# Kernel optimization log

Hardware: AMD Instinct MI355X
Metric: run time of the kernel (lower is better)

## Reference

```python
import jax, jax.numpy as jnp
import numpy as np

MAXDISP = 128  # from init_kwargs; 3*MAXDISP == 384 == enc0 in_planes

# 24 census offsets in a 5x5 window (center (2,2) skipped), order as in torch source
OFFSETS = [(0,0),(1,0),(2,0),(3,0),(4,0),(0,1),(1,1),(2,1),(3,1),(4,1),
           (0,2),(1,2),(3,2),(4,2),(0,3),(1,3),(2,3),(3,3),(4,3),
           (0,4),(1,4),(2,4),(3,4),(4,4)]


def rgb_to_ycbcr(img):
    # img: (n,3,h,w)
    r, g, b = img[:, 0], img[:, 1], img[:, 2]
    y = 0.299 * r + 0.587 * g + 0.114 * b
    cb = (b - y) * 0.564 + 0.5
    cr = (r - y) * 0.713 + 0.5
    return jnp.stack([y, cb, cr], axis=1)


def avg_pool2(x):
    n, c, h, w = x.shape
    return x.reshape(n, c, h // 2, 2, w // 2, 2).mean(axis=(3, 5))


def census5(img):
    # img: (n,1,h,w) float -> (n,1,h,w) int32, 24-bit census code, 2px zero border
    n, c, h, w = img.shape
    center = img[:, :, 2:h - 2, 2:w - 2]
    # (24, n, 1, h-4, w-4) boolean comparisons, exactly the torch offset order
    bits = jnp.stack([(img[:, :, v:v + h - 4, u:u + w - 4] >= center)
                      for (u, v) in OFFSETS], axis=0).astype(jnp.int32)
    weights = (2 ** jnp.arange(23, -1, -1)).astype(jnp.int32)  # census = census*2 + bit fold
    cen = jnp.tensordot(weights, bits, axes=1)
    return jnp.pad(cen, ((0, 0), (0, 0), (2, 2), (2, 2)))


def cost_volume(l, r, maxdisp, op):
    # l, r: (n,1,h,w). out[:, d, :, x] = op(l[x+d], r[x]) for x < w-d else 0,
    # matching torch's slice (left[d:w] vs right[0:w-d]) + right-pad with zeros.
    w = l.shape[-1]
    xs = jnp.arange(w)

    def per_d(d):
        l_sh = jnp.roll(l, -d, axis=-1)          # l_sh[..., x] = l[..., x+d] (wrapped part masked)
        c = op(l_sh, r)
        return jnp.where(xs < w - d, c, jnp.zeros_like(c))

    cv = jax.vmap(per_d)(jnp.arange(maxdisp))    # (D, n, 1, h, w)
    return cv[:, :, 0].transpose(1, 0, 2, 3)     # (n, D, h, w)


def setup_inputs() -> dict:
    key = jax.random.key(0)
    k1, k2 = jax.random.split(key)
    left = jax.random.uniform(k1, (2, 3, 384, 1280), dtype=jnp.float32)
    right = jax.random.uniform(k2, (2, 3, 384, 1280), dtype=jnp.float32)
    return {"left": left, "right": right}


def reference(left, right):
    # FDSCS front-end: half-res YCbCr, census+Hamming on Y, abs-diff on Cb/Cr, unify
    lp, rp = avg_pool2(left), avg_pool2(right)
    lyuv, ryuv = rgb_to_ycbcr(lp), rgb_to_ycbcr(rp)

    lc = census5(lyuv[:, 0:1])
    rc = census5(ryuv[:, 0:1])
    # Hamming distance = popcount of 24-bit XOR (codes < 2^24, so popcount == 24-bit loop)
    ham = cost_volume(lc, rc, MAXDISP,
                      lambda a, b: jax.lax.population_count(jnp.bitwise_xor(a, b))
                      ).astype(jnp.float32)
    u = cost_volume(lyuv[:, 1:2], ryuv[:, 1:2], MAXDISP, lambda a, b: jnp.abs(a - b))
    v = cost_volume(lyuv[:, 2:3], ryuv[:, 2:3], MAXDISP, lambda a, b: jnp.abs(a - b))

    # Unify_size normalization constants from torch source
    y_n = (ham - 11.08282948) / 0.1949711
    u_n = (u - 0.02175535) / 35.91432953
    v_n = (v - 0.02679042) / 26.79782867
    return jnp.concatenate([y_n, u_n, v_n], axis=1)  # (n, 3*MAXDISP, h/2, w/2)
```

## Files before the change

kernel.cpp:

```cpp
#include <hip/hip_runtime.h>

#define H   384
#define W   1280
#define PH  192
#define PW  640
#define PP  (PH*PW)

typedef float f32x4 __attribute__((ext_vector_type(4)));
typedef int   i32x4 __attribute__((ext_vector_type(4)));

__global__ __launch_bounds__(256) void pool_ycbcr_kernel(
    const float* __restrict__ left, const float* __restrict__ right,
    float* __restrict__ yp, float* __restrict__ cbp, float* __restrict__ crp)
{
    int tid = blockIdx.x * blockDim.x + threadIdx.x;
    if (tid >= 4 * PP) return;
    int p   = tid / PP;
    int rem = tid - p * PP;
    int y   = rem / PW;
    int x   = rem - y * PW;

    const float* src = (p < 2 ? left : right) + (size_t)(p & 1) * 3 * H * W;

    float pc[3];
#pragma unroll
    for (int c = 0; c < 3; ++c) {
        const float* ch = src + (size_t)c * H * W + (size_t)(2 * y) * W + 2 * x;
        float2 a = *(const float2*)ch;
        float2 b = *(const float2*)(ch + W);
        float s = __fadd_rn(__fadd_rn(__fadd_rn(a.x, a.y), b.x), b.y);
        pc[c] = __fmul_rn(s, 0.25f);
    }
    float yv = __fadd_rn(__fadd_rn(__fmul_rn(0.299f, pc[0]),
                                   __fmul_rn(0.587f, pc[1])),
                         __fmul_rn(0.114f, pc[2]));
    float cb = __fadd_rn(__fmul_rn(__fsub_rn(pc[2], yv), 0.564f), 0.5f);
    float cr = __fadd_rn(__fmul_rn(__fsub_rn(pc[0], yv), 0.713f), 0.5f);

    yp[tid]  = yv;
    cbp[tid] = cb;
    crp[tid] = cr;
}

__global__ __launch_bounds__(256) void census_kernel(
    const float* __restrict__ yp, int* __restrict__ cen)
{
    int tid = blockIdx.x * blockDim.x + threadIdx.x;
    if (tid >= 4 * PP) return;
    int p   = tid / PP;
    int rem = tid - p * PP;
    int y   = rem / PW;
    int x   = rem - y * PW;

    int code = 0;
    if (y >= 2 && y < PH - 2 && x >= 2 && x < PW - 2) {
        const float* base = yp + (size_t)p * PP;
        float c = base[y * PW + x];
        int bit = 23;
#pragma unroll
        for (int v = 0; v < 5; ++v) {
#pragma unroll
            for (int u = 0; u < 5; ++u) {
                if (u == 2 && v == 2) continue;
                float nb = base[(y - 2 + v) * PW + (x - 2 + u)];
                code |= (nb >= c ? 1 : 0) << bit;
                --bit;
            }
        }
    }
    cen[tid] = code;
}

__global__ __launch_bounds__(256) void costvol_kernel(
    const float* __restrict__ cbp, const float* __restrict__ crp,
    const int* __restrict__ cen, float* __restrict__ out)
{
    const float m1 = 11.08282948f, i1 = 1.0f / 0.1949711f;
    const float m2 = 0.02175535f,  i2 = 1.0f / 35.91432953f;
    const float m3 = 0.02679042f,  i3 = 1.0f / 26.79782867f;

    int b  = (blockIdx.x & 7) * 768 + (blockIdx.x >> 3);

    int yt = b & 7;
    int t  = b >> 3;
    int n  = t / 384;
    int ch = t - n * 384;
    int g  = ch >> 7;
    int d  = ch & 127;
    int nvalid = PW - d;
    int y0 = yt * 24;
    int s  = d & 3;
    int dal = d - s;
    const int tid = threadIdx.x;

    f32x4* ob = (f32x4*)(out + (((size_t)(n * 384 + ch)) * PH + y0) * PW);

    if (g == 0) {
        const float c0 = (0.0f - m1) * i1;
        const int* L = cen + (size_t)n * PP;
        const int* R = cen + (size_t)(2 + n) * PP;
#pragma unroll 5
        for (int k = 0; k < 15; ++k) {
            int i  = tid + 256 * k;
            int yy = i / 160;
            int x0 = (i - yy * 160) * 4;
            int row = (y0 + yy) * PW;
            i32x4 rv = *(const i32x4*)(R + row + x0);
            const int* Lp = L + row + x0 + dal;
            i32x4 A  = *(const i32x4*)(Lp);
            i32x4 Bv = *(const i32x4*)(Lp + 4);
            int e0, e1, e2, e3;
            if      (s == 0) { e0 = A.x;  e1 = A.y;  e2 = A.z;  e3 = A.w;  }
            else if (s == 1) { e0 = A.y;  e1 = A.z;  e2 = A.w;  e3 = Bv.x; }
            else if (s == 2) { e0 = A.z;  e1 = A.w;  e2 = Bv.x; e3 = Bv.y; }
            else             { e0 = A.w;  e1 = Bv.x; e2 = Bv.y; e3 = Bv.z; }
            f32x4 ov;
            ov.x = (x0 + 0 < nvalid) ? ((float)__popc(e0 ^ rv.x) - m1) * i1 : c0;
            ov.y = (x0 + 1 < nvalid) ? ((float)__popc(e1 ^ rv.y) - m1) * i1 : c0;
            ov.z = (x0 + 2 < nvalid) ? ((float)__popc(e2 ^ rv.z) - m1) * i1 : c0;
            ov.w = (x0 + 3 < nvalid) ? ((float)__popc(e3 ^ rv.w) - m1) * i1 : c0;
            __builtin_nontemporal_store(ov, ob + i);
        }
    } else {
        const float m  = (g == 1) ? m2 : m3;
        const float iv = (g == 1) ? i2 : i3;
        const float c0 = (0.0f - m) * iv;
        const float* P = (g == 1) ? cbp : crp;
        const float* L = P + (size_t)n * PP;
        const float* R = P + (size_t)(2 + n) * PP;
#pragma unroll 5
        for (int k = 0; k < 15; ++k) {
            int i  = tid + 256 * k;
            int yy = i / 160;
            int x0 = (i - yy * 160) * 4;
            int row = (y0 + yy) * PW;
            f32x4 rv = *(const f32x4*)(R + row + x0);
            const float* Lp = L + row + x0 + dal;
            f32x4 A  = *(const f32x4*)(Lp);
            f32x4 Bv = *(const f32x4*)(Lp + 4);
            float e0, e1, e2, e3;
            if      (s == 0) { e0 = A.x;  e1 = A.y;  e2 = A.z;  e3 = A.w;  }
            else if (s == 1) { e0 = A.y;  e1 = A.z;  e2 = A.w;  e3 = Bv.x; }
            else if (s == 2) { e0 = A.z;  e1 = A.w;  e2 = Bv.x; e3 = Bv.y; }
            else             { e0 = A.w;  e1 = Bv.x; e2 = Bv.y; e3 = Bv.z; }
            f32x4 ov;
            ov.x = (x0 + 0 < nvalid) ? (fabsf(e0 - rv.x) - m) * iv : c0;
            ov.y = (x0 + 1 < nvalid) ? (fabsf(e1 - rv.y) - m) * iv : c0;
            ov.z = (x0 + 2 < nvalid) ? (fabsf(e2 - rv.z) - m) * iv : c0;
            ov.w = (x0 + 3 < nvalid) ? (fabsf(e3 - rv.w) - m) * iv : c0;
            __builtin_nontemporal_store(ov, ob + i);
        }
    }
}

extern "C" void kernel_launch(void* const* d_in, const int* in_sizes, int n_in,
                              void* d_out, int out_size, void* d_ws, size_t ws_size,
                              hipStream_t stream)
{
    const float* left  = (const float*)d_in[0];
    const float* right = (const float*)d_in[1];

    float* ws  = (float*)d_ws;
    float* yp  = ws;
    float* cbp = ws + 4 * PP;
    float* crp = ws + 8 * PP;
    int*   cen = (int*)(ws + 12 * PP);

    int threads = 256;
    int blocksAB = (4 * PP + threads - 1) / threads;

    pool_ycbcr_kernel<<<blocksAB, threads, 0, stream>>>(left, right, yp, cbp, crp);
    census_kernel<<<blocksAB, threads, 0, stream>>>(yp, cen);

    int blocksC = 2 * 384 * 8;
    costvol_kernel<<<blocksC, threads, 0, stream>>>(cbp, crp, cen, (float*)d_out);
}
```

Before: 89.11 us.

## Stage one image row in LDS and sweep 64 disparities per block

The cost-volume kernel now assigns each block one image row, one channel group and half the disparity range. It stages the left and right rows in shared memory and computes 64 disparity planes from them, instead of reloading global data for every disparity. This is meant to cut redundant global and L2 reads. In exchange the output stores are scattered across 64 planes per block, and LDS reads at unaligned offsets may bank-conflict. The kernel is dominated by output writes, so the gain may be limited.

Measured after the change: 89.19 us. No clear change (+0.1%).

```diff
diff --git a/kernel.cpp b/kernel.cpp
--- a/kernel.cpp
+++ b/kernel.cpp
@@ -79,76 +79,79 @@
     const float m2 = 0.02175535f,  i2 = 1.0f / 35.91432953f;
     const float m3 = 0.02679042f,  i3 = 1.0f / 26.79782867f;
 
-    int b  = (blockIdx.x & 7) * 768 + (blockIdx.x >> 3);
+    int b   = blockIdx.x;
+    int n   = b / 1152;
+    int r   = b - n * 1152;
+    int g   = r / 384;
+    int r2  = r - g * 384;
+    int row = r2 >> 1;
+    int dh  = r2 & 1;
 
-    int yt = b & 7;
-    int t  = b >> 3;
-    int n  = t / 384;
-    int ch = t - n * 384;
-    int g  = ch >> 7;
-    int d  = ch & 127;
-    int nvalid = PW - d;
-    int y0 = yt * 24;
-    int s  = d & 3;
-    int dal = d - s;
-    const int tid = threadIdx.x;
+    __shared__ int Ls[776];
+    __shared__ int Rs[640];
 
-    f32x4* ob = (f32x4*)(out + (((size_t)(n * 384 + ch)) * PH + y0) * PW);
+    const int* Lplane;
+    const int* Rplane;
+    if (g == 0)      { Lplane = cen + (size_t)n * PP;
+                       Rplane = cen + (size_t)(2 + n) * PP; }
+    else if (g == 1) { Lplane = (const int*)(cbp + (size_t)n * PP);
+                       Rplane = (const int*)(cbp + (size_t)(2 + n) * PP); }
+    else             { Lplane = (const int*)(crp + (size_t)n * PP);
+                       Rplane = (const int*)(crp + (size_t)(2 + n) * PP); }
+
+    const i32x4* Lg4 = (const i32x4*)(Lplane + row * PW);
+    const i32x4* Rg4 = (const i32x4*)(Rplane + row * PW);
+
+    const int t = threadIdx.x;
+    for (int j = t; j < 320; j += 256) {
+        if (j < 160) *(i32x4*)&Ls[j * 4]         = Lg4[j];
+        else         *(i32x4*)&Rs[(j - 160) * 4] = Rg4[j - 160];
+    }
+    __syncthreads();
+
+    float* outb = out + ((size_t)(n * 384 + g * 128 + dh * 64) * PH + row) * PW;
 
     if (g == 0) {
         const float c0 = (0.0f - m1) * i1;
-        const int* L = cen + (size_t)n * PP;
-        const int* R = cen + (size_t)(2 + n) * PP;
-#pragma unroll 5
-        for (int k = 0; k < 15; ++k) {
-            int i  = tid + 256 * k;
-            int yy = i / 160;
-            int x0 = (i - yy * 160) * 4;
-            int row = (y0 + yy) * PW;
-            i32x4 rv = *(const i32x4*)(R + row + x0);
-            const int* Lp = L + row + x0 + dal;
-            i32x4 A  = *(const i32x4*)(Lp);
-            i32x4 Bv = *(const i32x4*)(Lp + 4);
-            int e0, e1, e2, e3;
-            if      (s == 0) { e0 = A.x;  e1 = A.y;  e2 = A.z;  e3 = A.w;  }
-            else if (s == 1) { e0 = A.y;  e1 = A.z;  e2 = A.w;  e3 = Bv.x; }
-            else if (s == 2) { e0 = A.z;  e1 = A.w;  e2 = Bv.x; e3 = Bv.y; }
-            else             { e0 = A.w;  e1 = Bv.x; e2 = Bv.y; e3 = Bv.z; }
+#pragma unroll 4
+        for (int idx = t; idx < 64 * 160; idx += 256) {
+            int dd = idx / 160;
+            int q  = idx - dd * 160;
+            int x0 = q * 4;
+            int d  = dh * 64 + dd;
+            int nvalid = PW - d;
+            i32x4 rv = *(const i32x4*)&Rs[x0];
+            int base = x0 + d;
+            int e0 = Ls[base], e1 = Ls[base + 1], e2 = Ls[base + 2], e3 = Ls[base + 3];
             f32x4 ov;
             ov.x = (x0 + 0 < nvalid) ? ((float)__popc(e0 ^ rv.x) - m1) * i1 : c0;
             ov.y = (x0 + 1 < nvalid) ? ((float)__popc(e1 ^ rv.y) - m1) * i1 : c0;
             ov.z = (x0 + 2 < nvalid) ? ((float)__popc(e2 ^ rv.z) - m1) * i1 : c0;
             ov.w = (x0 + 3 < nvalid) ? ((float)__popc(e3 ^ rv.w) - m1) * i1 : c0;
-            __builtin_nontemporal_store(ov, ob + i);
+            __builtin_nontemporal_store(ov, (f32x4*)(outb + (size_t)dd * PP + x0));
         }
     } else {
         const float m  = (g == 1) ? m2 : m3;
         const float iv = (g == 1) ? i2 : i3;
         const float c0 = (0.0f - m) * iv;
-        const float* P = (g == 1) ? cbp : crp;
-        const float* L = P + (size_t)n * PP;
-        const float* R = P + (size_t)(2 + n) * PP;
-#pragma unroll 5
-        for (int k = 0; k < 15; ++k) {
-            int i  = tid + 256 * k;
-            int yy = i / 160;
-            int x0 = (i - yy * 160) * 4;
-            int row = (y0 + yy) * PW;
-            f32x4 rv = *(const f32x4*)(R + row + x0);
-            const float* Lp = L + row + x0 + dal;
-            f32x4 A  = *(const f32x4*)(Lp);
-            f32x4 Bv = *(const f32x4*)(Lp + 4);
-            float e0, e1, e2, e3;
-            if      (s == 0) { e0 = A.x;  e1 = A.y;  e2 = A.z;  e3 = A.w;  }
-            else if (s == 1) { e0 = A.y;  e1 = A.z;  e2 = A.w;  e3 = Bv.x; }
-            else if (s == 2) { e0 = A.z;  e1 = A.w;  e2 = Bv.x; e3 = Bv.y; }
-            else             { e0 = A.w;  e1 = Bv.x; e2 = Bv.y; e3 = Bv.z; }
+        const float* Lf = (const float*)Ls;
+        const float* Rf = (const float*)Rs;
+#pragma unroll 4
+        for (int idx = t; idx < 64 * 160; idx += 256) {
+            int dd = idx / 160;
+            int q  = idx - dd * 160;
+            int x0 = q * 4;
+            int d  = dh * 64 + dd;
+            int nvalid = PW - d;
+            f32x4 rv = *(const f32x4*)&Rf[x0];
+            int base = x0 + d;
+            float e0 = Lf[base], e1 = Lf[base + 1], e2 = Lf[base + 2], e3 = Lf[base + 3];
             f32x4 ov;
             ov.x = (x0 + 0 < nvalid) ? (fabsf(e0 - rv.x) - m) * iv : c0;
             ov.y = (x0 + 1 < nvalid) ? (fabsf(e1 - rv.y) - m) * iv : c0;
             ov.z = (x0 + 2 < nvalid) ? (fabsf(e2 - rv.z) - m) * iv : c0;
             ov.w = (x0 + 3 < nvalid) ? (fabsf(e3 - rv.w) - m) * iv : c0;
-            __builtin_nontemporal_store(ov, ob + i);
+            __builtin_nontemporal_store(ov, (f32x4*)(outb + (size_t)dd * PP + x0));
         }
     }
 }
@@ -172,6 +175,6 @@
     pool_ycbcr_kernel<<<blocksAB, threads, 0, stream>>>(left, right, yp, cbp, crp);
     census_kernel<<<blocksAB, threads, 0, stream>>>(yp, cen);
 
-    int blocksC = 2 * 384 * 8;
+    int blocksC = 2 * 3 * 192 * 2;
     costvol_kernel<<<blocksC, threads, 0, stream>>>(cbp, crp, cen, (float*)d_out);
 }
```

## Assign one full output plane per block with 320-thread rows

Applied to the files above, without the earlier changes.

Restructures the cost-volume kernel so each block processes an entire output plane (two rows per iteration using 320 threads) instead of a 24-row tile. It replaces nontemporal stores with plain stores and skips the second left load when the disparity is 4-aligned. This aims to cut per-block index arithmetic and redundant loads. The trade-off is far fewer blocks (768) and less latency hiding. Dropping the nontemporal hint may also pollute caches on a write-bound kernel.

After: 99.07 us. 1.11x slower.

```diff
diff --git a/kernel.cpp b/kernel.cpp
--- a/kernel.cpp
+++ b/kernel.cpp
@@ -71,7 +71,7 @@
     cen[tid] = code;
 }
 
-__global__ __launch_bounds__(256) void costvol_kernel(
+__global__ __launch_bounds__(320) void costvol_kernel(
     const float* __restrict__ cbp, const float* __restrict__ crp,
     const int* __restrict__ cen, float* __restrict__ out)
 {
@@ -79,47 +79,47 @@
     const float m2 = 0.02175535f,  i2 = 1.0f / 35.91432953f;
     const float m3 = 0.02679042f,  i3 = 1.0f / 26.79782867f;
 
-    int b  = (blockIdx.x & 7) * 768 + (blockIdx.x >> 3);
-
-    int yt = b & 7;
-    int t  = b >> 3;
-    int n  = t / 384;
-    int ch = t - n * 384;
+    int plane = (blockIdx.x & 7) * 96 + (blockIdx.x >> 3);
+    int n  = plane / 384;
+    int ch = plane - n * 384;
     int g  = ch >> 7;
     int d  = ch & 127;
     int nvalid = PW - d;
-    int y0 = yt * 24;
-    int s  = d & 3;
+    int s   = d & 3;
     int dal = d - s;
-    const int tid = threadIdx.x;
 
-    f32x4* ob = (f32x4*)(out + (((size_t)(n * 384 + ch)) * PH + y0) * PW);
+    const int t    = threadIdx.x;
+    const int roff = t / 160;
+    const int x0   = (t - roff * 160) * 4;
+
+    float* ob = out + (size_t)plane * PP;
 
     if (g == 0) {
         const float c0 = (0.0f - m1) * i1;
         const int* L = cen + (size_t)n * PP;
         const int* R = cen + (size_t)(2 + n) * PP;
-#pragma unroll 5
-        for (int k = 0; k < 15; ++k) {
-            int i  = tid + 256 * k;
-            int yy = i / 160;
-            int x0 = (i - yy * 160) * 4;
-            int row = (y0 + yy) * PW;
+#pragma unroll 4
+        for (int i = 0; i < 96; ++i) {
+            int row = (2 * i + roff) * PW;
             i32x4 rv = *(const i32x4*)(R + row + x0);
             const int* Lp = L + row + x0 + dal;
-            i32x4 A  = *(const i32x4*)(Lp);
-            i32x4 Bv = *(const i32x4*)(Lp + 4);
             int e0, e1, e2, e3;
-            if      (s == 0) { e0 = A.x;  e1 = A.y;  e2 = A.z;  e3 = A.w;  }
-            else if (s == 1) { e0 = A.y;  e1 = A.z;  e2 = A.w;  e3 = Bv.x; }
-            else if (s == 2) { e0 = A.z;  e1 = A.w;  e2 = Bv.x; e3 = Bv.y; }
-            else             { e0 = A.w;  e1 = Bv.x; e2 = Bv.y; e3 = Bv.z; }
+            if (s == 0) {
+                i32x4 A = *(const i32x4*)Lp;
+                e0 = A.x; e1 = A.y; e2 = A.z; e3 = A.w;
+            } else {
+                i32x4 A  = *(const i32x4*)Lp;
+                i32x4 Bv = *(const i32x4*)(Lp + 4);
+                if      (s == 1) { e0 = A.y;  e1 = A.z;  e2 = A.w;  e3 = Bv.x; }
+                else if (s == 2) { e0 = A.z;  e1 = A.w;  e2 = Bv.x; e3 = Bv.y; }
+                else             { e0 = A.w;  e1 = Bv.x; e2 = Bv.y; e3 = Bv.z; }
+            }
             f32x4 ov;
             ov.x = (x0 + 0 < nvalid) ? ((float)__popc(e0 ^ rv.x) - m1) * i1 : c0;
             ov.y = (x0 + 1 < nvalid) ? ((float)__popc(e1 ^ rv.y) - m1) * i1 : c0;
             ov.z = (x0 + 2 < nvalid) ? ((float)__popc(e2 ^ rv.z) - m1) * i1 : c0;
             ov.w = (x0 + 3 < nvalid) ? ((float)__popc(e3 ^ rv.w) - m1) * i1 : c0;
-            __builtin_nontemporal_store(ov, ob + i);
+            *(f32x4*)(ob + row + x0) = ov;
         }
     } else {
         const float m  = (g == 1) ? m2 : m3;
@@ -128,27 +128,28 @@
         const float* P = (g == 1) ? cbp : crp;
         const float* L = P + (size_t)n * PP;
         const float* R = P + (size_t)(2 + n) * PP;
-#pragma unroll 5
-        for (int k = 0; k < 15; ++k) {
-            int i  = tid + 256 * k;
-            int yy = i / 160;
-            int x0 = (i - yy * 160) * 4;
-            int row = (y0 + yy) * PW;
+#pragma unroll 4
+        for (int i = 0; i < 96; ++i) {
+            int row = (2 * i + roff) * PW;
             f32x4 rv = *(const f32x4*)(R + row + x0);
             const float* Lp = L + row + x0 + dal;
-            f32x4 A  = *(const f32x4*)(Lp);
-            f32x4 Bv = *(const f32x4*)(Lp + 4);
             float e0, e1, e2, e3;
-            if      (s == 0) { e0 = A.x;  e1 = A.y;  e2 = A.z;  e3 = A.w;  }
-            else if (s == 1) { e0 = A.y;  e1 = A.z;  e2 = A.w;  e3 = Bv.x; }
-            else if (s == 2) { e0 = A.z;  e1 = A.w;  e2 = Bv.x; e3 = Bv.y; }
-            else             { e0 = A.w;  e1 = Bv.x; e2 = Bv.y; e3 = Bv.z; }
+            if (s == 0) {
+                f32x4 A = *(const f32x4*)Lp;
+                e0 = A.x; e1 = A.y; e2 = A.z; e3 = A.w;
+            } else {
+                f32x4 A  = *(const f32x4*)Lp;
+                f32x4 Bv = *(const f32x4*)(Lp + 4);
+                if      (s == 1) { e0 = A.y;  e1 = A.z;  e2 = A.w;  e3 = Bv.x; }
+                else if (s == 2) { e0 = A.z;  e1 = A.w;  e2 = Bv.x; e3 = Bv.y; }
+                else             { e0 = A.w;  e1 = Bv.x; e2 = Bv.y; e3 = Bv.z; }
+            }
             f32x4 ov;
             ov.x = (x0 + 0 < nvalid) ? (fabsf(e0 - rv.x) - m) * iv : c0;
             ov.y = (x0 + 1 < nvalid) ? (fabsf(e1 - rv.y) - m) * iv : c0;
             ov.z = (x0 + 2 < nvalid) ? (fabsf(e2 - rv.z) - m) * iv : c0;
             ov.w = (x0 + 3 < nvalid) ? (fabsf(e3 - rv.w) - m) * iv : c0;
-            __builtin_nontemporal_store(ov, ob + i);
+            *(f32x4*)(ob + row + x0) = ov;
         }
     }
 }
@@ -172,6 +173,6 @@
     pool_ycbcr_kernel<<<blocksAB, threads, 0, stream>>>(left, right, yp, cbp, crp);
     census_kernel<<<blocksAB, threads, 0, stream>>>(yp, cen);
 
-    int blocksC = 2 * 384 * 8;
-    costvol_kernel<<<blocksC, threads, 0, stream>>>(cbp, crp, cen, (float*)d_out);
+    int blocksC = 2 * 384;
+    costvol_kernel<<<blocksC, 320, 0, stream>>>(cbp, crp, cen, (float*)d_out);
 }
```
